# Kernel optimization log

Hardware: AMD Instinct MI355X
Metric: run time of the kernel (lower is better)

## Reference

```python
import jax, jax.numpy as jnp
import numpy as np

G, NPG, EPG = 128, 256, 4096   # graphs, nodes/graph, edges/graph
N, E = G * NPG, G * EPG
IN, H = 64, 64
RATIO = 0.5
K = int(RATIO * EPG)  # edges reserved per graph


def setup_inputs() -> dict:
    key = jax.random.key(0)
    ks = jax.random.split(key, 20)
    x = jax.random.normal(ks[0], (N, IN), dtype=jnp.float32)
    # per-graph random edges (block-diagonal structure, contiguous per graph)
    src = jax.random.randint(ks[1], (G, EPG), 0, NPG)
    dst = jax.random.randint(ks[2], (G, EPG), 0, NPG)
    offs = (jnp.arange(G) * NPG)[:, None]
    edge_index = jnp.stack([(src + offs).reshape(-1), (dst + offs).reshape(-1)]).astype(jnp.int64)
    edge_attr = jax.random.uniform(ks[3], (E,), dtype=jnp.float32)
    batch = jnp.repeat(jnp.arange(G), NPG).astype(jnp.int64)

    def w(k, shape):
        return jax.random.normal(k, shape, dtype=jnp.float32) * 0.1
    return {
        'x': x, 'edge_attr': edge_attr,
        'W11': w(ks[4], (H, IN)), 'b11': w(ks[5], (H,)), 'W12': w(ks[6], (H, IN)),
        'W13': w(ks[7], (H, IN)), 'b13': w(ks[8], (H,)),
        'W21': w(ks[9], (H, H)), 'b21': w(ks[10], (H,)), 'W22': w(ks[11], (H, H)),
        'W23': w(ks[12], (H, H)), 'b23': w(ks[13], (H,)),
        'Wm1': w(ks[14], (4 * H, 2 * H)), 'bm1': w(ks[15], (4 * H,)),
        'Wm2': w(ks[16], (1, 4 * H)), 'bm2': w(ks[17], (1,)),
        'edge_index': edge_index, 'batch': batch,
    }


def leconv(x, row, col, ew, W1, b1, W2, W3, b3):
    # PyG LEConv: out_i = sum_{(j->i)} e_ji * (lin1(x_j) - lin2(x_i)) + lin3(x_i)
    a = x @ W1.T + b1          # lin1 (bias)
    b = x @ W2.T               # lin2 (no bias)
    msg = ew[:, None] * (a[row] - b[col])            # [E, H]
    agg = jax.ops.segment_sum(msg, col, num_segments=x.shape[0])
    return agg + x @ W3.T + b3


def relabel_edges(ei):
    # torch relabel(): map used nodes to compact ids; fixed-shape variant returns
    # the remapped edge_index plus a node-presence mask instead of gathering x.
    present = jnp.zeros((N,), jnp.int32).at[ei.reshape(-1)].set(1)
    nid = jnp.where(present == 1, jnp.cumsum(present) - 1, -1)
    return nid[ei], present


def reference(x, edge_attr, W11, b11, W12, W13, b13, W21, b21, W22, W23, b23,
              Wm1, bm1, Wm2, bm2, edge_index, batch):
    row, col = edge_index[0], edge_index[1]
    h = jax.nn.relu(leconv(x, row, col, edge_attr, W11, b11, W12, W13, b13))
    h = leconv(h, row, col, edge_attr, W21, b21, W22, W23, b23)
    # edge scoring MLP on concat(x[row], x[col])
    edge_rep = jnp.concatenate([h[row], h[col]], axis=-1)       # [E, 2H]
    score = (jax.nn.relu(edge_rep @ Wm1.T + bm1) @ Wm2.T + bm2).reshape(-1)  # [E]
    # per-graph top-k split (graphs are uniform -> static shapes)
    s = score.reshape(G, EPG)
    order = jnp.argsort(-s, axis=1)
    keep, drop = order[:, :K], order[:, K:]
    causal_w = jnp.take_along_axis(s, keep, axis=1).reshape(-1)
    conf_w = -jnp.take_along_axis(s, drop, axis=1).reshape(-1)
    eoffs = (jnp.arange(G) * EPG)[:, None]
    kg = (keep + eoffs).reshape(-1)
    dg = (drop + eoffs).reshape(-1)
    causal_ei = edge_index[:, kg]
    conf_ei = edge_index[:, dg]
    causal_ei_rel, causal_mask = relabel_edges(causal_ei)
    conf_ei_rel, conf_mask = relabel_edges(conf_ei)
    out = jnp.concatenate([score, causal_w, conf_w])            # [2E]
    return out, causal_ei_rel, conf_ei_rel, causal_mask, conf_mask
```

## Files before the change

### kernel.cpp

```cpp
#include <hip/hip_runtime.h>
#include <cstddef>

#define G_    128
#define NPG_  256
#define EPG_  4096
#define NN_   32768
#define EE_   524288
#define KK_   2048
#define GK_   262144

#define O_CW  524288
#define O_DW  786432
#define O_CEI 1048576
#define O_FEI 1572864
#define O_CM  2097152
#define O_DM  2129920

typedef float v4f __attribute__((ext_vector_type(4)));
typedef unsigned long long u64;

struct BiasCfg {
  const float* b[8];
};

__device__ __forceinline__ void cswap(u64& a, u64& b, bool d) {
  u64 hi = a > b ? a : b, lo = a > b ? b : a;
  a = d ? hi : lo;
  b = d ? lo : hi;
}

__device__ __forceinline__ void gemm_wt_body(const float* __restrict__ in, int istride,
                                             const float* __restrict__ WT, int wstride,
                                             const BiasCfg& bc, int ncb,
                                             float* __restrict__ out, int ostride,
                                             int bx, float* xT) {
  const int tid = threadIdx.x;
  const int r0 = bx * 64;
#pragma unroll
  for (int it = 0; it < 16; ++it) {
    int idx = tid + it * 256;
    int rr = idx >> 6, kk = idx & 63;
    xT[kk * 68 + rr] = in[(r0 + rr) * istride + kk];
  }
  __syncthreads();
  const int c4 = (tid & 15) * 4;
  const int r4 = (tid >> 4) * 4;
  for (int cb = 0; cb < ncb; ++cb) {
    const float* wp = WT + cb * 64 + c4;
    const float* bp = bc.b[cb];
    float acc[4][4] = {};
#pragma unroll
    for (int k = 0; k < 64; ++k) {
      float4 xv = *(const float4*)&xT[k * 68 + r4];
      float4 wv = *(const float4*)&wp[(size_t)k * wstride];
      float xr[4] = {xv.x, xv.y, xv.z, xv.w};
      float wc[4] = {wv.x, wv.y, wv.z, wv.w};
#pragma unroll
      for (int a = 0; a < 4; ++a)
#pragma unroll
        for (int b = 0; b < 4; ++b)
          acc[a][b] = fmaf(xr[a], wc[b], acc[a][b]);
    }
    float bx4[4] = {0.f, 0.f, 0.f, 0.f};
    if (bp) {
      float4 bb = *(const float4*)&bp[c4];
      bx4[0] = bb.x; bx4[1] = bb.y; bx4[2] = bb.z; bx4[3] = bb.w;
    }
#pragma unroll
    for (int ri = 0; ri < 4; ++ri) {
      v4f st;
      st.x = acc[ri][0] + bx4[0];
      st.y = acc[ri][1] + bx4[1];
      st.z = acc[ri][2] + bx4[2];
      st.w = acc[ri][3] + bx4[3];
      __builtin_nontemporal_store(st, (v4f*)&out[(r0 + r4 + ri) * ostride + cb * 64 + c4]);
    }
    __syncthreads();
  }
}

__global__ __launch_bounds__(256, 4) void gemm_wt(const float* __restrict__ in, int istride,
                                                  const float* __restrict__ WT, int wstride,
                                                  BiasCfg bc, int ncb,
                                                  float* __restrict__ out, int ostride) {
  __shared__ float xT[64 * 68];
  gemm_wt_body(in, istride, WT, wstride, bc, ncb, out, ostride, blockIdx.x, xT);
}

__global__ __launch_bounds__(256) void prep_kernel(const float* __restrict__ Wm1,
                                                   const float* __restrict__ W11, const float* __restrict__ W12,
                                                   const float* __restrict__ W13,
                                                   const float* __restrict__ W21, const float* __restrict__ W22,
                                                   const float* __restrict__ W23,
                                                   float* __restrict__ WmT, float* __restrict__ W1T,
                                                   float* __restrict__ W2T, int* __restrict__ masks) {
  const int b = blockIdx.x;
  const int tid = threadIdx.x;
  if (b < 64) {
    const int k = b;
#pragma unroll
    for (int t = 0; t < 2; ++t) {
      int j = t * 256 + tid;
      int row = j & 255;
      int koff = (j < 256) ? 0 : 64;
      WmT[k * 512 + j] = Wm1[row * 128 + koff + k];
    }
  } else if (b < 80) {
    const int kb = (b - 64) * 4;
    if (tid < 192) {
      int cb = tid >> 6, c = tid & 63;
      const float* Wsrc = (cb == 0) ? W11 : (cb == 1) ? W12 : W13;
#pragma unroll
      for (int s = 0; s < 4; ++s) {
        int k = kb + s;
        W1T[k * 192 + tid] = Wsrc[c * 64 + k];
      }
    }
  } else if (b < 96) {
    const int kb = (b - 80) * 4;
    if (tid < 192) {
      int cb = tid >> 6, c = tid & 63;
      const float* Wsrc = (cb == 0) ? W21 : (cb == 1) ? W22 : W23;
#pragma unroll
      for (int s = 0; s < 4; ++s) {
        int k = kb + s;
        W2T[k * 192 + tid] = Wsrc[c * 64 + k];
      }
    }
  } else {
    int idx = (b - 96) * 1024 + tid * 4;
    int4 z = {0, 0, 0, 0};
    *(int4*)&masks[idx] = z;
  }
}

__global__ __launch_bounds__(256) void build_dense(const int* __restrict__ ei, const float* __restrict__ ea,
                                                   float* __restrict__ MT, float* __restrict__ Wc) {
  __shared__ float acc[NPG_ * 128];
  const int tid = threadIdx.x;
  const int g = blockIdx.x >> 1;
  const int c0 = (blockIdx.x & 1) * 128;
  const int gbase = g * NPG_;
  const size_t mbase = (size_t)g << 16;
  for (int i = tid * 4; i < NPG_ * 128; i += 1024) {
    float4 z = {0.f, 0.f, 0.f, 0.f};
    *(float4*)&acc[i] = z;
  }
  __syncthreads();
  const int ebase = g * EPG_;
#pragma unroll
  for (int it = 0; it < 16; ++it) {
    int e = ebase + it * 256 + tid;
    int r = ei[e] - gbase;
    int ch = ei[EE_ + e] - gbase - c0;
    float w = ea[e];
    if ((unsigned)ch < 128u) atomicAdd(&acc[r * 128 + ch], w);
  }
  __syncthreads();
  for (int i = tid; i < NPG_ * 32; i += 256) {
    int r = i >> 5, c4 = (i & 31) * 4;
    *(float4*)&MT[mbase + (size_t)r * 256 + c0 + c4] = *(const float4*)&acc[r * 128 + c4];
  }
  if (tid < 128) {
    float s = 0.f;
    for (int r = 0; r < NPG_; ++r) s += acc[r * 128 + tid];
    Wc[gbase + c0 + tid] = s;
  }
}

__global__ __launch_bounds__(256) void mm_agg(const float* __restrict__ MT, const float* __restrict__ buf,
                                              const float* __restrict__ Wc, float* __restrict__ hout,
                                              int do_relu) {
  __shared__ float Ms[64 * 72];
  __shared__ float As[64 * 72];
  const int tid = threadIdx.x;
  const int g = blockIdx.x >> 2;
  const int c0 = (blockIdx.x & 3) * 64;
  const int gbase = g * NPG_;
  const size_t mbase = (size_t)g << 16;
  const int c4 = (tid >> 4) * 4;
  const int k4 = (tid & 15) * 4;
  float acc[4][4] = {};
  for (int kc = 0; kc < 4; ++kc) {
#pragma unroll
    for (int it = 0; it < 16; ++it) {
      int idx = tid + it * 256;
      int rr = idx >> 6, cc = idx & 63;
      Ms[rr * 72 + cc] = MT[mbase + (size_t)(kc * 64 + rr) * 256 + c0 + cc];
      As[rr * 72 + cc] = buf[(gbase + kc * 64 + rr) * 192 + cc];
    }
    __syncthreads();
#pragma unroll
    for (int r = 0; r < 64; ++r) {
      float4 mv = *(const float4*)&Ms[r * 72 + c4];
      float4 av = *(const float4*)&As[r * 72 + k4];
      float mr[4] = {mv.x, mv.y, mv.z, mv.w};
      float ak[4] = {av.x, av.y, av.z, av.w};
#pragma unroll
      for (int ci = 0; ci < 4; ++ci)
#pragma unroll
        for (int ki = 0; ki < 4; ++ki)
          acc[ci][ki] = fmaf(mr[ci], ak[ki], acc[ci][ki]);
    }
    __syncthreads();
  }
#pragma unroll
  for (int ci = 0; ci < 4; ++ci) {
    int n = gbase + c0 + c4 + ci;
    float wcn = Wc[n];
    float4 b4 = *(const float4*)&buf[n * 192 + 64 + k4];
    float4 cc4 = *(const float4*)&buf[n * 192 + 128 + k4];
    float4 st;
    st.x = acc[ci][0] - wcn * b4.x + cc4.x;
    st.y = acc[ci][1] - wcn * b4.y + cc4.y;
    st.z = acc[ci][2] - wcn * b4.z + cc4.z;
    st.w = acc[ci][3] - wcn * b4.w + cc4.w;
    if (do_relu) {
      st.x = fmaxf(st.x, 0.f); st.y = fmaxf(st.y, 0.f);
      st.z = fmaxf(st.z, 0.f); st.w = fmaxf(st.w, 0.f);
    }
    *(float4*)&hout[n * 64 + k4] = st;
  }
}

__global__ __launch_bounds__(256, 4) void score_v4(const float* __restrict__ pq, const int* __restrict__ ei,
                                                   const float* __restrict__ wm2, const float* __restrict__ bm2,
                                                   float* __restrict__ out) {
  __shared__ float Ps[256 * 20];
  __shared__ float Qs[256 * 20];
  const int tid = threadIdx.x;
  const int g = blockIdx.x & 127;
  const int quarter = blockIdx.x >> 7;
  const int gbase = g * NPG_;
  const int ebase = g * EPG_ + quarter * 1024;
  int rl[4], cl[4];
  float acc[4] = {};
#pragma unroll
  for (int j = 0; j < 4; ++j) {
    int e = ebase + j * 256 + tid;
    rl[j] = (ei[e] - gbase) * 20;
    cl[j] = (ei[EE_ + e] - gbase) * 20;
  }
  for (int t = 0; t < 16; ++t) {
    __syncthreads();
#pragma unroll
    for (int it = 0; it < 4; ++it) {
      int idx = tid + it * 256;
      int node = idx >> 2, k4 = (idx & 3) * 4;
      const float* src = &pq[(size_t)(gbase + node) * 512 + t * 16 + k4];
      *(float4*)&Ps[node * 20 + k4] = *(const float4*)src;
      *(float4*)&Qs[node * 20 + k4] = *(const float4*)(src + 256);
    }
    __syncthreads();
#pragma unroll
    for (int k4 = 0; k4 < 16; k4 += 4) {
      float4 w4 = *(const float4*)&wm2[t * 16 + k4];
#pragma unroll
      for (int j = 0; j < 4; ++j) {
        float4 p = *(const float4*)&Ps[rl[j] + k4];
        float4 q = *(const float4*)&Qs[cl[j] + k4];
        acc[j] = fmaf(w4.x, fmaxf(p.x + q.x, 0.f), acc[j]);
        acc[j] = fmaf(w4.y, fmaxf(p.y + q.y, 0.f), acc[j]);
        acc[j] = fmaf(w4.z, fmaxf(p.z + q.z, 0.f), acc[j]);
        acc[j] = fmaf(w4.w, fmaxf(p.w + q.w, 0.f), acc[j]);
      }
    }
  }
  const float beta = bm2[0];
#pragma unroll
  for (int j = 0; j < 4; ++j) out[ebase + j * 256 + tid] = acc[j] + beta;
}

__global__ __launch_bounds__(1024) void sort_kernel(float* __restrict__ out, const int* __restrict__ ei,
                                                    int* __restrict__ kg, int* __restrict__ dg,
                                                    int* __restrict__ cmask, int* __restrict__ dmask) {
  __shared__ u64 keys[EPG_];
  const int g = blockIdx.x;
  const int tid = threadIdx.x;
  const int b = 4 * tid;
  u64 e[4];
  {
    float4 s4 = *(const float4*)&out[g * EPG_ + b];
    float sv[4] = {s4.x, s4.y, s4.z, s4.w};
#pragma unroll
    for (int s = 0; s < 4; ++s) {
      unsigned u = __float_as_uint(sv[s]);
      u = (u & 0x80000000u) ? ~u : (u | 0x80000000u);
      e[s] = ((u64)u << 32) | (unsigned)(~(b + s));
    }
  }
  cswap(e[0], e[1], true);
  cswap(e[2], e[3], false);
  {
    bool d = ((b & 4) == 0);
    cswap(e[0], e[2], d); cswap(e[1], e[3], d);
    cswap(e[0], e[1], d); cswap(e[2], e[3], d);
  }
  for (int k = 8; k <= EPG_; k <<= 1) {
    if (k >= 512) {
#pragma unroll
      for (int s = 0; s < 4; ++s) keys[b + s] = e[s];
      __syncthreads();
      for (int j = k >> 1; j >= 256; j >>= 1) {
        const int jm1 = j - 1;
        const int p0 = tid, p1 = tid + 1024;
        const int i0 = ((p0 & ~jm1) << 1) | (p0 & jm1);
        const int i1 = ((p1 & ~jm1) << 1) | (p1 & jm1);
        u64 a0 = keys[i0], b0 = keys[i0 + j];
        u64 a1 = keys[i1], b1 = keys[i1 + j];
        bool d0 = ((i0 & k) == 0), d1 = ((i1 & k) == 0);
        u64 hi0 = a0 > b0 ? a0 : b0, lo0 = a0 > b0 ? b0 : a0;
        u64 hi1 = a1 > b1 ? a1 : b1, lo1 = a1 > b1 ? b1 : a1;
        keys[i0]     = d0 ? hi0 : lo0;
        keys[i0 + j] = d0 ? lo0 : hi0;
        keys[i1]     = d1 ? hi1 : lo1;
        keys[i1 + j] = d1 ? lo1 : hi1;
        __syncthreads();
      }
#pragma unroll
      for (int s = 0; s < 4; ++s) e[s] = keys[b + s];
    }
    const bool d = ((tid & (k >> 2)) == 0);
    for (int j = (k >> 1) > 128 ? 128 : (k >> 1); j >= 4; j >>= 1) {
      const int delta = j >> 2;
      const bool lower = ((tid & delta) == 0);
      const bool keepmax = (lower == d);
#pragma unroll
      for (int s = 0; s < 4; ++s) {
        u64 p = __shfl_xor(e[s], delta);
        u64 mx = e[s] > p ? e[s] : p;
        u64 mn = e[s] > p ? p : e[s];
        e[s] = keepmax ? mx : mn;
      }
    }
    cswap(e[0], e[2], d); cswap(e[1], e[3], d);
    cswap(e[0], e[1], d); cswap(e[2], e[3], d);
  }
#pragma unroll
  for (int s = 0; s < 4; ++s) {
    const int p = b + s;
    u64 kv = e[s];
    int i = (int)(~(unsigned)kv);
    unsigned hi = (unsigned)(kv >> 32);
    unsigned ub = (hi & 0x80000000u) ? (hi ^ 0x80000000u) : ~hi;
    float sc = __uint_as_float(ub);
    int ed = g * EPG_ + i;
    int r = ei[ed], c = ei[EE_ + ed];
    if (p < KK_) {
      out[O_CW + g * KK_ + p] = sc;
      kg[g * KK_ + p] = ed;
      cmask[r] = 1; cmask[c] = 1;
    } else {
      int q = p - KK_;
      out[O_DW + g * KK_ + q] = -sc;
      dg[g * KK_ + q] = ed;
      dmask[r] = 1; dmask[c] = 1;
    }
  }
}

__global__ __launch_bounds__(1024) void scan_kernel(const int* __restrict__ masks, int* __restrict__ nids) {
  const int which = blockIdx.x;
  const int* m = masks + which * NN_;
  int* nid = nids + which * NN_;
  const int tid = threadIdx.x;
  const int base = tid * 32;
  int local[32];
  int sum = 0;
#pragma unroll
  for (int j = 0; j < 32; ++j) { local[j] = m[base + j]; sum += local[j]; }
  __shared__ int ps[1024];
  ps[tid] = sum;
  __syncthreads();
  for (int off = 1; off < 1024; off <<= 1) {
    int v = (tid >= off) ? ps[tid - off] : 0;
    __syncthreads();
    ps[tid] += v;
    __syncthreads();
  }
  int run = ps[tid] - sum;
#pragma unroll
  for (int j = 0; j < 32; ++j) { run += local[j]; nid[base + j] = run - 1; }
}

__global__ __launch_bounds__(256) void finalize_kernel(const int* __restrict__ kg, const int* __restrict__ dg,
                                                       const int* __restrict__ ei,
                                                       const int* __restrict__ nid_c, const int* __restrict__ nid_d,
                                                       const int* __restrict__ cmask, const int* __restrict__ dmask,
                                                       float* __restrict__ out) {
  const int p = blockIdx.x * 256 + threadIdx.x;
  int e = kg[p];
  out[O_CEI + p]       = (float)nid_c[ei[e]];
  out[O_CEI + GK_ + p] = (float)nid_c[ei[EE_ + e]];
  int e2 = dg[p];
  out[O_FEI + p]       = (float)nid_d[ei[e2]];
  out[O_FEI + GK_ + p] = (float)nid_d[ei[EE_ + e2]];
  if (p < NN_) {
    out[O_CM + p] = (float)cmask[p];
    out[O_DM + p] = (float)dmask[p];
  }
}

extern "C" void kernel_launch(void* const* d_in, const int* in_sizes, int n_in,
                              void* d_out, int out_size, void* d_ws, size_t ws_size,
                              hipStream_t stream) {
  (void)in_sizes; (void)n_in; (void)out_size; (void)ws_size;
  const float* x   = (const float*)d_in[0];
  const float* ea  = (const float*)d_in[1];
  const float* W11 = (const float*)d_in[2];
  const float* b11 = (const float*)d_in[3];
  const float* W12 = (const float*)d_in[4];
  const float* W13 = (const float*)d_in[5];
  const float* b13 = (const float*)d_in[6];
  const float* W21 = (const float*)d_in[7];
  const float* b21 = (const float*)d_in[8];
  const float* W22 = (const float*)d_in[9];
  const float* W23 = (const float*)d_in[10];
  const float* b23 = (const float*)d_in[11];
  const float* Wm1 = (const float*)d_in[12];
  const float* bm1 = (const float*)d_in[13];
  const float* Wm2 = (const float*)d_in[14];
  const float* bm2 = (const float*)d_in[15];
  const int*   ei  = (const int*)d_in[16];
  float* out = (float*)d_out;
  float* ws  = (float*)d_ws;

  float* MT  = ws;
  float* Wc  = ws + 8388608;
  float* buf = ws + 8421376;
  float* pq  = ws;
  float* h_c = ws + 16777216;
  int* kg    = (int*)(ws + 18874368);
  int* dg    = kg + GK_;
  int* cmask = dg + GK_;
  int* dmask = cmask + NN_;
  int* nid_c = dmask + NN_;
  int* nid_d = nid_c + NN_;
  float* WmT = ws + 18874368;
  float* W1T = WmT + 32768;
  float* W2T = W1T + 12288;

  prep_kernel<<<160, 256, 0, stream>>>(Wm1, W11, W12, W13, W21, W22, W23, WmT, W1T, W2T, cmask);

  build_dense<<<256, 256, 0, stream>>>(ei, ea, MT, Wc);

  BiasCfg bc1{};
  bc1.b[0] = b11; bc1.b[1] = nullptr; bc1.b[2] = b13;
  gemm_wt<<<512, 256, 0, stream>>>(x, 64, W1T, 192, bc1, 3, buf, 192);

  mm_agg<<<512, 256, 0, stream>>>(MT, buf, Wc, h_c, 1);

  BiasCfg bc2{};
  bc2.b[0] = b21; bc2.b[1] = nullptr; bc2.b[2] = b23;
  gemm_wt<<<512, 256, 0, stream>>>(h_c, 64, W2T, 192, bc2, 3, buf, 192);

  mm_agg<<<512, 256, 0, stream>>>(MT, buf, Wc, h_c, 0);

  BiasCfg bc3{};
  for (int cb = 0; cb < 4; ++cb) { bc3.b[cb] = bm1 + cb * 64; bc3.b[cb + 4] = nullptr; }
  gemm_wt<<<512, 256, 0, stream>>>(h_c, 64, WmT, 512, bc3, 8, pq, 512);

  score_v4<<<512, 256, 0, stream>>>(pq, ei, Wm2, bm2, out);

  sort_kernel<<<G_, 1024, 0, stream>>>(out, ei, kg, dg, cmask, dmask);

  scan_kernel<<<2, 1024, 0, stream>>>(cmask, nid_c);

  finalize_kernel<<<GK_ / 256, 256, 0, stream>>>(kg, dg, ei, nid_c, nid_d, cmask, dmask, out);
}
```

Measured before the change: 329.1 us.

## Merge prep and dense-build kernels, retile GEMM, vectorize mm_agg tile loads

Folds the weight-transpose/mask-zero prep kernel and the dense adjacency build into a single launch, using the block index to pick the role, which saves one kernel launch. Changes the gemm_wt thread tile from 4x4 to 2x8, with two strided float4 weight loads per k. Switches the mm_agg shared-memory tile loads from scalar to float4. Because the fused kernel now reserves 128KB of shared memory for every block, the small prep blocks may occupy CUs less efficiently.

```diff
diff --git a/kernel.cpp b/kernel.cpp
--- a/kernel.cpp
+++ b/kernel.cpp
@@ -43,37 +43,42 @@
     xT[kk * 68 + rr] = in[(r0 + rr) * istride + kk];
   }
   __syncthreads();
-  const int c4 = (tid & 15) * 4;
-  const int r4 = (tid >> 4) * 4;
+  const int c8 = (tid & 7) * 4;
+  const int r2 = (tid >> 3) * 2;
   for (int cb = 0; cb < ncb; ++cb) {
-    const float* wp = WT + cb * 64 + c4;
+    const float* wp = WT + cb * 64;
     const float* bp = bc.b[cb];
-    float acc[4][4] = {};
+    float acc[2][8] = {};
 #pragma unroll
     for (int k = 0; k < 64; ++k) {
-      float4 xv = *(const float4*)&xT[k * 68 + r4];
-      float4 wv = *(const float4*)&wp[(size_t)k * wstride];
-      float xr[4] = {xv.x, xv.y, xv.z, xv.w};
-      float wc[4] = {wv.x, wv.y, wv.z, wv.w};
-#pragma unroll
-      for (int a = 0; a < 4; ++a)
-#pragma unroll
-        for (int b = 0; b < 4; ++b)
+      float2 xv = *(const float2*)&xT[k * 68 + r2];
+      float4 wv0 = *(const float4*)&wp[(size_t)k * wstride + c8];
+      float4 wv1 = *(const float4*)&wp[(size_t)k * wstride + c8 + 32];
+      float xr[2] = {xv.x, xv.y};
+      float wc[8] = {wv0.x, wv0.y, wv0.z, wv0.w, wv1.x, wv1.y, wv1.z, wv1.w};
+#pragma unroll
+      for (int a = 0; a < 2; ++a)
+#pragma unroll
+        for (int b = 0; b < 8; ++b)
           acc[a][b] = fmaf(xr[a], wc[b], acc[a][b]);
     }
-    float bx4[4] = {0.f, 0.f, 0.f, 0.f};
+    float bx8[8] = {0.f, 0.f, 0.f, 0.f, 0.f, 0.f, 0.f, 0.f};
     if (bp) {
-      float4 bb = *(const float4*)&bp[c4];
-      bx4[0] = bb.x; bx4[1] = bb.y; bx4[2] = bb.z; bx4[3] = bb.w;
-    }
-#pragma unroll
-    for (int ri = 0; ri < 4; ++ri) {
-      v4f st;
-      st.x = acc[ri][0] + bx4[0];
-      st.y = acc[ri][1] + bx4[1];
-      st.z = acc[ri][2] + bx4[2];
-      st.w = acc[ri][3] + bx4[3];
-      __builtin_nontemporal_store(st, (v4f*)&out[(r0 + r4 + ri) * ostride + cb * 64 + c4]);
+      float4 b0 = *(const float4*)&bp[c8];
+      float4 b1 = *(const float4*)&bp[c8 + 32];
+      bx8[0] = b0.x; bx8[1] = b0.y; bx8[2] = b0.z; bx8[3] = b0.w;
+      bx8[4] = b1.x; bx8[5] = b1.y; bx8[6] = b1.z; bx8[7] = b1.w;
+    }
+#pragma unroll
+    for (int a = 0; a < 2; ++a) {
+      float* orow = &out[(size_t)(r0 + r2 + a) * ostride + cb * 64];
+      v4f s0, s1;
+      s0.x = acc[a][0] + bx8[0]; s0.y = acc[a][1] + bx8[1];
+      s0.z = acc[a][2] + bx8[2]; s0.w = acc[a][3] + bx8[3];
+      s1.x = acc[a][4] + bx8[4]; s1.y = acc[a][5] + bx8[5];
+      s1.z = acc[a][6] + bx8[6]; s1.w = acc[a][7] + bx8[7];
+      __builtin_nontemporal_store(s0, (v4f*)&orow[c8]);
+      __builtin_nontemporal_store(s1, (v4f*)&orow[c8 + 32]);
     }
     __syncthreads();
   }
@@ -87,59 +92,60 @@
   gemm_wt_body(in, istride, WT, wstride, bc, ncb, out, ostride, blockIdx.x, xT);
 }
 
-__global__ __launch_bounds__(256) void prep_kernel(const float* __restrict__ Wm1,
-                                                   const float* __restrict__ W11, const float* __restrict__ W12,
-                                                   const float* __restrict__ W13,
-                                                   const float* __restrict__ W21, const float* __restrict__ W22,
-                                                   const float* __restrict__ W23,
-                                                   float* __restrict__ WmT, float* __restrict__ W1T,
-                                                   float* __restrict__ W2T, int* __restrict__ masks) {
+__global__ __launch_bounds__(256) void prep_build(const float* __restrict__ Wm1,
+                                                  const float* __restrict__ W11, const float* __restrict__ W12,
+                                                  const float* __restrict__ W13,
+                                                  const float* __restrict__ W21, const float* __restrict__ W22,
+                                                  const float* __restrict__ W23,
+                                                  float* __restrict__ WmT, float* __restrict__ W1T,
+                                                  float* __restrict__ W2T, int* __restrict__ masks,
+                                                  const int* __restrict__ ei, const float* __restrict__ ea,
+                                                  float* __restrict__ MT, float* __restrict__ Wc) {
+  __shared__ float acc[NPG_ * 128];
   const int b = blockIdx.x;
   const int tid = threadIdx.x;
-  if (b < 64) {
-    const int k = b;
-#pragma unroll
-    for (int t = 0; t < 2; ++t) {
-      int j = t * 256 + tid;
-      int row = j & 255;
-      int koff = (j < 256) ? 0 : 64;
-      WmT[k * 512 + j] = Wm1[row * 128 + koff + k];
-    }
-  } else if (b < 80) {
-    const int kb = (b - 64) * 4;
-    if (tid < 192) {
-      int cb = tid >> 6, c = tid & 63;
-      const float* Wsrc = (cb == 0) ? W11 : (cb == 1) ? W12 : W13;
-#pragma unroll
-      for (int s = 0; s < 4; ++s) {
-        int k = kb + s;
-        W1T[k * 192 + tid] = Wsrc[c * 64 + k];
-      }
-    }
-  } else if (b < 96) {
-    const int kb = (b - 80) * 4;
-    if (tid < 192) {
-      int cb = tid >> 6, c = tid & 63;
-      const float* Wsrc = (cb == 0) ? W21 : (cb == 1) ? W22 : W23;
-#pragma unroll
-      for (int s = 0; s < 4; ++s) {
-        int k = kb + s;
-        W2T[k * 192 + tid] = Wsrc[c * 64 + k];
-      }
-    }
-  } else {
-    int idx = (b - 96) * 1024 + tid * 4;
-    int4 z = {0, 0, 0, 0};
-    *(int4*)&masks[idx] = z;
-  }
-}
-
-__global__ __launch_bounds__(256) void build_dense(const int* __restrict__ ei, const float* __restrict__ ea,
-                                                   float* __restrict__ MT, float* __restrict__ Wc) {
-  __shared__ float acc[NPG_ * 128];
-  const int tid = threadIdx.x;
-  const int g = blockIdx.x >> 1;
-  const int c0 = (blockIdx.x & 1) * 128;
+  if (b < 160) {
+    if (b < 64) {
+      const int k = b;
+#pragma unroll
+      for (int t = 0; t < 2; ++t) {
+        int j = t * 256 + tid;
+        int row = j & 255;
+        int koff = (j < 256) ? 0 : 64;
+        WmT[k * 512 + j] = Wm1[row * 128 + koff + k];
+      }
+    } else if (b < 80) {
+      const int kb = (b - 64) * 4;
+      if (tid < 192) {
+        int cb = tid >> 6, c = tid & 63;
+        const float* Wsrc = (cb == 0) ? W11 : (cb == 1) ? W12 : W13;
+#pragma unroll
+        for (int s = 0; s < 4; ++s) {
+          int k = kb + s;
+          W1T[k * 192 + tid] = Wsrc[c * 64 + k];
+        }
+      }
+    } else if (b < 96) {
+      const int kb = (b - 80) * 4;
+      if (tid < 192) {
+        int cb = tid >> 6, c = tid & 63;
+        const float* Wsrc = (cb == 0) ? W21 : (cb == 1) ? W22 : W23;
+#pragma unroll
+        for (int s = 0; s < 4; ++s) {
+          int k = kb + s;
+          W2T[k * 192 + tid] = Wsrc[c * 64 + k];
+        }
+      }
+    } else {
+      int idx = (b - 96) * 1024 + tid * 4;
+      int4 z = {0, 0, 0, 0};
+      *(int4*)&masks[idx] = z;
+    }
+    return;
+  }
+  const int bb = b - 160;
+  const int g = bb >> 1;
+  const int c0 = (bb & 1) * 128;
   const int gbase = g * NPG_;
   const size_t mbase = (size_t)g << 16;
   for (int i = tid * 4; i < NPG_ * 128; i += 1024) {
@@ -183,11 +189,11 @@
   float acc[4][4] = {};
   for (int kc = 0; kc < 4; ++kc) {
 #pragma unroll
-    for (int it = 0; it < 16; ++it) {
+    for (int it = 0; it < 4; ++it) {
       int idx = tid + it * 256;
-      int rr = idx >> 6, cc = idx & 63;
-      Ms[rr * 72 + cc] = MT[mbase + (size_t)(kc * 64 + rr) * 256 + c0 + cc];
-      As[rr * 72 + cc] = buf[(gbase + kc * 64 + rr) * 192 + cc];
+      int rr = idx >> 4, c16 = (idx & 15) * 4;
+      *(float4*)&Ms[rr * 72 + c16] = *(const float4*)&MT[mbase + (size_t)(kc * 64 + rr) * 256 + c0 + c16];
+      *(float4*)&As[rr * 72 + c16] = *(const float4*)&buf[(gbase + kc * 64 + rr) * 192 + c16];
     }
     __syncthreads();
 #pragma unroll
@@ -440,9 +446,8 @@
   float* W1T = WmT + 32768;
   float* W2T = W1T + 12288;
 
-  prep_kernel<<<160, 256, 0, stream>>>(Wm1, W11, W12, W13, W21, W22, W23, WmT, W1T, W2T, cmask);
-
-  build_dense<<<256, 256, 0, stream>>>(ei, ea, MT, Wc);
+  prep_build<<<416, 256, 0, stream>>>(Wm1, W11, W12, W13, W21, W22, W23,
+                                      WmT, W1T, W2T, cmask, ei, ea, MT, Wc);
 
   BiasCfg bc1{};
   bc1.b[0] = b11; bc1.b[1] = nullptr; bc1.b[2] = b13;
```

After: 671.3 us. +104.0%, slower.
